# Kernel tuning notes

Measured on AMD Instinct MI355X. Metric: run time of the kernel, lower is better.

Reference implementation:

```python
import math
import jax, jax.numpy as jnp
import numpy as np

B = 2
TMAX = 1024
D = 1024
H = 16
DK = D // H
F = 4096
L = 2
CHUNK = 128
LEFT = 128
RIGHT = 32
EPS = 1e-5


def _build_mask(t_max, chunk, left, right):
    """Replicates EmformerEncoder.create_mask with audio_lens == t_max.
    Returns bool [T, T] where True = masked (disallowed), T = total_right + t_max."""
    num_chunks = math.ceil(t_max / chunk)
    ub = (num_chunks - 1) * right
    body = np.zeros((t_max, t_max), np.float32)
    mleft = np.zeros((t_max, ub), np.float32)
    mdiag = np.zeros((ub, ub), np.float32)
    mright = np.zeros((ub, t_max), np.float32)
    right_indexes = []
    for i in range(num_chunks):
        left_off = max(chunk * i - left, 0)
        start = chunk * i
        end = min(chunk * (i + 1), t_max)
        body[start:end, left_off:end] = 1
        if i == num_chunks - 1:
            break
        rem = t_max - (end + right)
        trl = right if rem >= 0 else t_max - end
        ri = len(right_indexes)
        mleft[start:start + chunk, ri:ri + trl] = 1
        mdiag[ri:ri + trl, ri:ri + trl] = 1
        mright[ri:ri + trl, left_off:end] = 1
        right_indexes += list(range(end, end + trl))
    rs = len(right_indexes)
    mleft = mleft[:, :rs]
    mdiag = mdiag[:rs, :rs]
    mright = mright[:rs, :]
    top = np.concatenate([mdiag, mright], axis=-1)
    bot = np.concatenate([mleft, body], axis=-1)
    m = np.concatenate([top, bot], axis=0)
    return m == 0  # True where attention is NOT allowed


def setup_inputs() -> dict:
    key = jax.random.key(0)
    ks = jax.random.split(key, 8)
    mask2d = _build_mask(TMAX, CHUNK, LEFT, RIGHT)  # [T, T]
    T = mask2d.shape[0]  # 1248
    w = lambda k, shape: jax.random.normal(k, shape, jnp.float32) * 0.02
    inp = {
        "input": jax.random.normal(ks[0], (B, T, D), jnp.float32),
        "ln_in_scale": jnp.ones((L, D), jnp.float32),
        "ln_in_bias": jnp.zeros((L, D), jnp.float32),
        "Wq": w(ks[1], (L, D, D)), "bq": jnp.zeros((L, D), jnp.float32),
        "Wk": w(ks[2], (L, D, D)), "bk": jnp.zeros((L, D), jnp.float32),
        "Wv": w(ks[3], (L, D, D)), "bv": jnp.zeros((L, D), jnp.float32),
        "ln1_scale": jnp.ones((L, D), jnp.float32),
        "ln1_bias": jnp.zeros((L, D), jnp.float32),
        "W1": w(ks[4], (L, D, F)), "b1": jnp.zeros((L, F), jnp.float32),
        "W2": w(ks[5], (L, F, D)), "b2": jnp.zeros((L, D), jnp.float32),
        "ln2_scale": jnp.ones((L, D), jnp.float32),
        "ln2_bias": jnp.zeros((L, D), jnp.float32),
        "mask": jnp.asarray(np.broadcast_to(mask2d[None, None], (B, 1, T, T)).copy()),
    }
    return inp


def _ln(x, scale, bias):
    m = jnp.mean(x, axis=-1, keepdims=True)
    v = jnp.mean(jnp.square(x - m), axis=-1, keepdims=True)
    return (x - m) * jax.lax.rsqrt(v + EPS) * scale + bias


def reference(input, ln_in_scale, ln_in_bias, Wq, bq, Wk, bk, Wv, bv,
              ln1_scale, ln1_bias, W1, b1, W2, b2, ln2_scale, ln2_bias, mask):
    x = input
    Bx, T, _ = x.shape
    scale = 1.0 / math.sqrt(DK)
    for l in range(L):
        h = _ln(x, ln_in_scale[l], ln_in_bias[l])  # pre-LN input (also residual base)
        q = (h @ Wq[l] + bq[l]).reshape(Bx, T, H, DK)
        k = (h @ Wk[l] + bk[l]).reshape(Bx, T, H, DK)
        v = (h @ Wv[l] + bv[l]).reshape(Bx, T, H, DK)
        scores = jnp.einsum('bqhd,bkhd->bhqk', q, k) * scale  # [B,H,T,T]
        scores = jnp.where(mask, -jnp.inf, scores)
        probs = jax.nn.softmax(scores, axis=-1)
        probs = jnp.where(mask, 0.0, probs)  # dropout_attn=0 -> identity
        o = jnp.einsum('bhqk,bkhd->bqhd', probs, v).reshape(Bx, T, D)
        attn_out = o + h
        y = _ln(attn_out, ln1_scale[l], ln1_bias[l])
        y = y @ W1[l] + b1[l]          # note: no activation in original code
        y = y @ W2[l] + b2[l] + attn_out
        x = _ln(y, ln2_scale[l], ln2_bias[l])
    return x
```

## Files before the change

kernel.cpp:

```cpp
#include <hip/hip_runtime.h>
#include <stdint.h>

typedef __attribute__((ext_vector_type(8))) short short8;
typedef __attribute__((ext_vector_type(4))) float f32x4;

#define DEV __device__ __forceinline__

DEV float bits2f(uint32_t u){ union{uint32_t u;float f;}v; v.u=u; return v.f; }
DEV float bf1(uint16_t s){ return bits2f(((uint32_t)s)<<16); }
DEV uint16_t f2bf(float f){ union{float f;uint32_t u;}v; v.f=f; uint32_t u=v.u;
  return (uint16_t)((u + 0x7fffu + ((u>>16)&1u))>>16); }
DEV uint16_t f2h(float a){ union{_Float16 h; uint16_t u;}v; v.h=(_Float16)a; return v.u; }
DEV float h2f(uint16_t s){ union{uint16_t u; _Float16 h;}v; v.u=s; return (float)v.h; }

DEV float ldval(const float* p, size_t i){ return p[i]; }
DEV float ldval(const uint16_t* p, size_t i){ return bf1(p[i]); }
DEV void stval(float* p, size_t i, float v){ p[i]=v; }
DEV void stval(uint16_t* p, size_t i, float v){ p[i]=f2bf(v); }

DEV void async16(const void* g, void* l){
#if __has_builtin(__builtin_amdgcn_global_load_lds)
  __builtin_amdgcn_global_load_lds((const __attribute__((address_space(1))) void*)g,
                                   (__attribute__((address_space(3))) void*)l, 16, 0, 0);
#else
  int lane = threadIdx.x & 63;
  *(uint4*)((char*)l + lane*16) = *(const uint4*)((const char*)g);
#endif
}

template<int TM, int TN, bool SPLIT>
__global__ __launch_bounds__(256) void gemm_t(
    const uint16_t* __restrict__ A, const uint16_t* __restrict__ Bt,
    const float* __restrict__ bias, void* __restrict__ Cout,
    int N, int K, int kchunk, int gm, int gx, int gy, int nG,
    const float* __restrict__ Tsrc1, const float* __restrict__ Tsrc2,
    uint16_t* __restrict__ Tdst1, uint16_t* __restrict__ Tdst2) {
  __shared__ uint16_t sA[3][TM*32];
  __shared__ uint16_t sB[3][TN*32];
  constexpr int LPS = TM/64 + TN/64;
  const int tid = threadIdx.x;
  const int lin = blockIdx.y*gx + blockIdx.x;

  if (lin >= nG) {
    float (*t)[33] = (float(*)[33])&sA[0][0];
    int tt = lin - nG;
    const float* src; uint16_t* dst; int R, C, c0, r0;
    if (tt < 4096) { src = Tsrc1; dst = Tdst1; R = 1024; C = 4096;
                     c0 = (tt&127)*32; r0 = (tt>>7)*32; }
    else { tt -= 4096; src = Tsrc2; dst = Tdst2; R = 4096; C = 1024;
           c0 = (tt&31)*32; r0 = (tt>>5)*32; }
    const int tx = tid&31, ty = tid>>5;
    #pragma unroll
    for (int i=0;i<4;i++) t[ty+8*i][tx] = src[(size_t)(r0+ty+8*i)*C + c0+tx];
    __syncthreads();
    #pragma unroll
    for (int i=0;i<4;i++) dst[(size_t)(c0+ty+8*i)*R + r0+tx] = f2bf(t[tx][ty+8*i]);
    return;
  }

  int mt_, nt_;
  if (gm > 0) {
    const int xcd = lin & 7, idx = lin >> 3;
    const int RM = gy / gm;
    const int RN = (gx * gm) >> 3;
    const int rm = xcd % gm, rn = xcd / gm;
    mt_ = rm*RM + idx % RM;
    nt_ = rn*RN + idx / RM;
  } else {
    const int q8 = (gx*gy) >> 3;
    const int swz = (lin & 7)*q8 + (lin >> 3);
    mt_ = swz % gy; nt_ = swz / gy;
  }
  const int m0 = mt_*TM, n0 = nt_*TN;
  const int kb = SPLIT ? blockIdx.z*kchunk : 0;
  const int kend = SPLIT ? kb + kchunk : K;
  const int wid = tid>>6, lane = tid&63;
  constexpr int WM = TM/2, MT = WM/16;
  constexpr int WN = TN/2, NT = WN/16;
  const int wm = (wid&1)*WM, wn = (wid>>1)*WN;
  f32x4 acc[MT][NT];
  #pragma unroll
  for (int a=0;a<MT;a++)
    #pragma unroll
    for (int b=0;b<NT;b++) acc[a][b] = (f32x4){0.f,0.f,0.f,0.f};
  const int lrow = lane>>2;
  const int lcol = (((lane&3) ^ ((lrow>>1)&3)))*8;
  const int fr = lane&15, fc = lane>>4;
  const int rsw = (fc ^ ((fr>>1)&3))*8;

  auto stage = [&](int buf, int k0) {
    #pragma unroll
    for (int j = 0; j < TM/64; ++j) {
      int r0 = wid*(TM/4) + j*16;
      async16(A + (size_t)(m0+r0+lrow)*K + k0 + lcol, &sA[buf][r0*32]);
    }
    #pragma unroll
    for (int j = 0; j < TN/64; ++j) {
      int r0 = wid*(TN/4) + j*16;
      async16(Bt + (size_t)(n0+r0+lrow)*K + k0 + lcol, &sB[buf][r0*32]);
    }
  };

  const int niter = (kend - kb) >> 5;
  stage(0, kb);
  if (niter > 1) stage(1, kb + 32);
  int cur = 0;
  for (int it = 0; it < niter; ++it) {
    if (it+1 < niter) {
      if constexpr (LPS == 4)      asm volatile("s_waitcnt vmcnt(4)" ::: "memory");
      else if constexpr (LPS == 3) asm volatile("s_waitcnt vmcnt(3)" ::: "memory");
      else                         asm volatile("s_waitcnt vmcnt(2)" ::: "memory");
    } else {
      asm volatile("s_waitcnt vmcnt(0)" ::: "memory");
    }
    __builtin_amdgcn_s_barrier();
    __builtin_amdgcn_sched_barrier(0);
    if (it+2 < niter) {
      int b2 = cur+2; if (b2>=3) b2-=3;
      stage(b2, kb + (it+2)*32);
    }
    short8 af[MT], bfv[NT];
    #pragma unroll
    for (int t=0;t<MT;t++) af[t] = *(const short8*)&sA[cur][(wm + t*16 + fr)*32 + rsw];
    #pragma unroll
    for (int t=0;t<NT;t++) bfv[t] = *(const short8*)&sB[cur][(wn + t*16 + fr)*32 + rsw];
    #pragma unroll
    for (int mt=0;mt<MT;mt++)
      #pragma unroll
      for (int nt=0;nt<NT;nt++)
        acc[mt][nt] = __builtin_amdgcn_mfma_f32_16x16x32_bf16(af[mt], bfv[nt], acc[mt][nt], 0,0,0);
    if (++cur == 3) cur = 0;
  }
  const int cl = lane&15, rl = (lane>>4)*4;
  if (SPLIT) {
    float* Pz = (float*)Cout + (size_t)blockIdx.z*2560*N;
    #pragma unroll
    for (int nt=0;nt<NT;nt++) {
      int n = n0 + wn + nt*16 + cl;
      #pragma unroll
      for (int mt=0;mt<MT;mt++)
        #pragma unroll
        for (int r=0;r<4;r++)
          Pz[(size_t)(m0 + wm + mt*16 + rl + r)*N + n] = acc[mt][nt][r];
    }
  } else {
    uint16_t* C = (uint16_t*)Cout;
    #pragma unroll
    for (int nt=0;nt<NT;nt++) {
      int n = n0 + wn + nt*16 + cl;
      float bv = bias ? bias[n] : 0.f;
      #pragma unroll
      for (int mt=0;mt<MT;mt++)
        #pragma unroll
        for (int r=0;r<4;r++)
          C[(size_t)(m0 + wm + mt*16 + rl + r)*N + n] = f2bf(acc[mt][nt][r] + bv);
    }
  }
}

template<typename TI, typename TO>
DEV void ln_body(int row, int tid, const TI* x, const float* sc, const float* bi,
                 TO* out, float* red) {
  const size_t base = (size_t)row*1024 + tid*4;
  float v0=ldval(x,base), v1=ldval(x,base+1), v2=ldval(x,base+2), v3=ldval(x,base+3);
  float s = v0+v1+v2+v3;
  float sq = v0*v0+v1*v1+v2*v2+v3*v3;
  #pragma unroll
  for (int off=32; off; off>>=1){ s += __shfl_xor(s,off); sq += __shfl_xor(sq,off); }
  int wid=tid>>6, lane=tid&63;
  if (lane==0){ red[wid]=s; red[4+wid]=sq; }
  __syncthreads();
  s = red[0]+red[1]+red[2]+red[3]; sq = red[4]+red[5]+red[6]+red[7];
  float mean = s*(1.f/1024.f);
  float inv  = rsqrtf(sq*(1.f/1024.f) - mean*mean + 1e-5f);
  int c = tid*4;
  stval(out, base,   (v0-mean)*inv*sc[c]   + bi[c]);
  stval(out, base+1, (v1-mean)*inv*sc[c+1] + bi[c+1]);
  stval(out, base+2, (v2-mean)*inv*sc[c+2] + bi[c+2]);
  stval(out, base+3, (v3-mean)*inv*sc[c+3] + bi[c+3]);
}

template<typename TI, typename TO>
__global__ __launch_bounds__(256) void ln_k(const TI* __restrict__ x,
    const float* __restrict__ sc, const float* __restrict__ bi,
    TO* __restrict__ out) {
  __shared__ float red[8];
  ln_body<TI,TO>(blockIdx.x, threadIdx.x, x, sc, bi, out, red);
}

template<typename TO>
__global__ __launch_bounds__(256) void ln2_fused(const float* __restrict__ P,
    const float* __restrict__ b2, const uint16_t* __restrict__ resid,
    const float* __restrict__ sc, const float* __restrict__ bi,
    TO* __restrict__ out) {
  const int row = blockIdx.x, tid = threadIdx.x;
  const size_t base = (size_t)row*1024 + tid*4;
  float4 p0 = *(const float4*)(P + base);
  float4 p1 = *(const float4*)(P + (size_t)2560*1024 + base);
  int c = tid*4;
  float v0 = p0.x+p1.x+b2[c]  +bf1(resid[base]);
  float v1 = p0.y+p1.y+b2[c+1]+bf1(resid[base+1]);
  float v2 = p0.z+p1.z+b2[c+2]+bf1(resid[base+2]);
  float v3 = p0.w+p1.w+b2[c+3]+bf1(resid[base+3]);
  float s = v0+v1+v2+v3;
  float sq = v0*v0+v1*v1+v2*v2+v3*v3;
  #pragma unroll
  for (int off=32; off; off>>=1){ s += __shfl_xor(s,off); sq += __shfl_xor(sq,off); }
  __shared__ float red[8];
  int wid=tid>>6, lane=tid&63;
  if (lane==0){ red[wid]=s; red[4+wid]=sq; }
  __syncthreads();
  s = red[0]+red[1]+red[2]+red[3]; sq = red[4]+red[5]+red[6]+red[7];
  float mean = s*(1.f/1024.f);
  float inv  = rsqrtf(sq*(1.f/1024.f) - mean*mean + 1e-5f);
  stval(out, base,   (v0-mean)*inv*sc[c]   + bi[c]);
  stval(out, base+1, (v1-mean)*inv*sc[c+1] + bi[c+1]);
  stval(out, base+2, (v2-mean)*inv*sc[c+2] + bi[c+2]);
  stval(out, base+3, (v3-mean)*inv*sc[c+3] + bi[c+3]);
}

__global__ __launch_bounds__(256) void attn_fused(
    const uint32_t* __restrict__ qkv32, const uint16_t* __restrict__ hres,
    uint16_t* __restrict__ attn_out) {
  const int blk = blockIdx.x;
  const int qg = (blk>>3)&3;
  const int g  = (blk&7) + ((blk>>5)<<3);
  const int ci = g&7, hh = (g>>3)&15, bb = g>>7;
  const int sum_cnt = (ci<7)?32:0;
  const int bstart = (ci>=1)?128*(ci-1):0;
  const int bend = (ci==7)?1024:128*(ci+1);
  const int nk = sum_cnt + (bend - bstart);
  const int rowbase = bb*1248;
  const int tid = threadIdx.x, wid = tid>>6, lane = tid&63;
  const int fr = lane&15, fc = lane>>4;

  __shared__ __attribute__((aligned(16))) uint16_t sm[30848];
  uint16_t* SP16 = sm;
  uint16_t* Q16 = sm + 20736;
  uint32_t* QD  = (uint32_t*)Q16;
  uint16_t* V16 = sm + 11840;
  uint32_t* VD  = (uint32_t*)(sm + 11840);

  for (int idx = tid; idx < 40*8; idx += 256) {
    int j = idx>>3, q4 = idx&7;
    int ql = qg*40 + j;
    int tq = (ql<32) ? (32*ci+ql) : (224+128*ci+ql-32);
    *(uint4*)&QD[j*36 + q4*4] =
      *(const uint4*)&qkv32[(size_t)(rowbase+tq)*1536 + hh*32 + q4*4];
  }
  __syncthreads();

  const int n_mt = nk>>4;
  const int qoff[3] = {0,16,24};
  f32x4 accs[5][3];
  #pragma unroll
  for (int a=0;a<5;a++)
    #pragma unroll
    for (int b=0;b<3;b++) accs[a][b] = (f32x4){0.f,0.f,0.f,0.f};
  __builtin_amdgcn_s_setprio(1);
  #pragma unroll
  for (int ks=0; ks<2; ++ks) {
    short8 bq_[3];
    #pragma unroll
    for (int nt=0;nt<3;nt++)
      bq_[nt] = *(const short8*)&Q16[(qoff[nt]+fr)*72 + ks*32 + fc*8];
    #pragma unroll
    for (int t=0;t<5;t++) {
      int mt = wid + 4*t;
      if (mt < n_mt) {
        int mrow = mt*16 + fr;
        int tk = (mrow < sum_cnt) ? (32*ci + mrow) : (224 + bstart + mrow - sum_cnt);
        short8 a_ = *(const short8*)&qkv32[(size_t)(rowbase+tk)*1536 + 512 + hh*32 + ks*16 + fc*4];
        #pragma unroll
        for (int nt=0;nt<3;nt++)
          accs[t][nt] = __builtin_amdgcn_mfma_f32_16x16x32_bf16(a_, bq_[nt], accs[t][nt], 0,0,0);
      }
    }
  }
  __builtin_amdgcn_s_setprio(0);
  __syncthreads();

  #pragma unroll
  for (int t=0;t<5;t++) {
    int mt = wid + 4*t;
    if (mt < n_mt) {
      #pragma unroll
      for (int nt=0;nt<3;nt++) {
        int q = qoff[nt] + fr;
        #pragma unroll
        for (int r=0;r<4;r++)
          SP16[q*296 + mt*16 + fc*4 + r] = f2h(accs[t][nt][r]*0.125f);
      }
    }
  }
  for (int idx = tid; idx < nk*8; idx += 256) {
    int j = idx>>3, q4 = idx&7;
    int tk = (j < sum_cnt) ? (32*ci + j) : (224 + bstart + (j - sum_cnt));
    uint4 w = *(const uint4*)&qkv32[(size_t)(rowbase+tk)*1536 + 1024 + hh*32 + q4*4];
    uint32_t* dst = &VD[j*33 + q4*4];
    dst[0]=w.x; dst[1]=w.y; dst[2]=w.z; dst[3]=w.w;
  }
  __syncthreads();

  for (int i=0;i<10;i++) {
    int row = wid*10 + i;
    float v[5];
    #pragma unroll
    for (int g2=0;g2<5;g2++){ int k=g2*64+lane; v[g2] = (k<nk) ? h2f(SP16[row*296+k]) : -1e30f; }
    float mx = fmaxf(fmaxf(fmaxf(v[0],v[1]),fmaxf(v[2],v[3])),v[4]);
    #pragma unroll
    for (int off=32; off; off>>=1) mx = fmaxf(mx, __shfl_xor(mx,off));
    float p[5], sum=0.f;
    #pragma unroll
    for (int g2=0;g2<5;g2++){ p[g2] = __expf(v[g2]-mx); if (g2*64+lane>=nk) p[g2]=0.f; sum+=p[g2]; }
    #pragma unroll
    for (int off=32; off; off>>=1) sum += __shfl_xor(sum,off);
    float inv = 1.f/sum;
    #pragma unroll
    for (int g2=0;g2<5;g2++){ int k=g2*64+lane; if (k<nk) SP16[row*296+k] = f2bf(p[g2]*inv); }
  }
  __syncthreads();

  const int nkt = nk>>5;
  f32x4 acco[3];
  #pragma unroll
  for (int t=0;t<3;t++) acco[t] = (f32x4){0.f,0.f,0.f,0.f};
  const uint16_t* vcol = V16 + wid*16 + fr;
  __builtin_amdgcn_s_setprio(1);
  for (int kt=0; kt<nkt; ++kt) {
    short8 bv_;
    #pragma unroll
    for (int j=0;j<8;j++) bv_[j] = (short)vcol[(kt*32 + fc*8 + j)*66];
    #pragma unroll
    for (int t=0;t<3;t++) {
      short8 a_ = *(const short8*)&SP16[(qoff[t]+fr)*296 + kt*32 + fc*8];
      acco[t] = __builtin_amdgcn_mfma_f32_16x16x32_bf16(a_, bv_, acco[t], 0,0,0);
    }
  }
  __builtin_amdgcn_s_setprio(0);
  #pragma unroll
  for (int t=0;t<3;t++) {
    #pragma unroll
    for (int r=0;r<4;r++) {
      bool vq = true;
      if (ci==7 && qg==0 && (qoff[t]+fc*4+r)<32) vq = false;
      if (vq) {
        int qll = qg*40 + qoff[t] + fc*4 + r;
        int tq = (qll<32) ? (32*ci+qll) : (224+128*ci+qll-32);
        size_t addr = (size_t)(rowbase+tq)*1024 + hh*64 + wid*16 + fr;
        attn_out[addr] = f2bf(acco[t][r] + bf1(hres[addr]));
      }
    }
  }
}

__global__ void prep_k(const float* __restrict__ Wq, const float* __restrict__ Wk,
                       const float* __restrict__ Wv, const float* __restrict__ bq,
                       const float* __restrict__ bk, const float* __restrict__ bv,
                       uint16_t* __restrict__ wt_qkv, float* __restrict__ bqkv,
                       const void* __restrict__ lnx, int lnx_f32,
                       const float* __restrict__ lnsc, const float* __restrict__ lnbi,
                       uint16_t* __restrict__ lnout) {
  __shared__ float t[32][33];
  const int blk = blockIdx.x;
  const int tx = threadIdx.x, ty = threadIdx.y;
  if (blk >= 3084) {
    int row = blk - 3084;
    int tid = ty*32 + tx;
    float* red = &t[0][0];
    if (lnx_f32) ln_body<float,uint16_t>((int)row, tid, (const float*)lnx, lnsc, lnbi, lnout, red);
    else         ln_body<uint16_t,uint16_t>((int)row, tid, (const uint16_t*)lnx, lnsc, lnbi, lnout, red);
    return;
  }
  if (blk >= 3072) {
    int i = (blk-3072)*256 + ty*32 + tx;
    bqkv[i] = (i<1024) ? bq[i] : ((i<2048) ? bk[i-1024] : bv[i-2048]);
    return;
  }
  int w = blk>>10, tt = blk&1023;
  const float* src = (w==0)?Wq:((w==1)?Wk:Wv);
  uint16_t* dst = wt_qkv + (size_t)w*1048576;
  const int R = 1024, C = 1024;
  const int c0 = (tt&31)*32, r0 = (tt>>5)*32;
  #pragma unroll
  for (int i=0;i<4;i++) t[ty+8*i][tx] = src[(size_t)(r0+ty+8*i)*C + c0+tx];
  __syncthreads();
  #pragma unroll
  for (int i=0;i<4;i++) dst[(size_t)(c0+ty+8*i)*R + r0+tx] = f2bf(t[tx][ty+8*i]);
}

extern "C" void kernel_launch(void* const* d_in, const int* in_sizes, int n_in,
                              void* d_out, int out_size, void* d_ws, size_t ws_size,
                              hipStream_t stream) {
  const float* input  = (const float*)d_in[0];
  const float* lnin_s = (const float*)d_in[1];
  const float* lnin_b = (const float*)d_in[2];
  const float* Wq = (const float*)d_in[3];
  const float* bq = (const float*)d_in[4];
  const float* Wk = (const float*)d_in[5];
  const float* bk = (const float*)d_in[6];
  const float* Wv = (const float*)d_in[7];
  const float* bv = (const float*)d_in[8];
  const float* ln1_s = (const float*)d_in[9];
  const float* ln1_b = (const float*)d_in[10];
  const float* W1 = (const float*)d_in[11];
  const float* b1 = (const float*)d_in[12];
  const float* W2 = (const float*)d_in[13];
  const float* b2 = (const float*)d_in[14];
  const float* ln2_s = (const float*)d_in[15];
  const float* ln2_b = (const float*)d_in[16];

  char* ws = (char*)d_ws;
  uint16_t* wt_qkv = (uint16_t*)(ws + 0);
  uint16_t* wt_w1  = (uint16_t*)(ws + 6291456);
  uint16_t* wt_w2  = (uint16_t*)(ws + 14680064);
  float*    bqkv   = (float*)   (ws + 23068672);
  uint16_t* hbuf   = (uint16_t*)(ws + 23080960);
  uint16_t* qkvb   = (uint16_t*)(ws + 28323840);
  uint16_t* attnb  = (uint16_t*)(ws + 44052480);
  uint16_t* zbuf   = (uint16_t*)(ws + 49295360);
  float*    pbuf   = (float*)   (ws + 54538240);
  uint16_t* y1b    = hbuf;
  uint16_t* x1b    = zbuf;

  const uint16_t* xcur_bf = x1b;
  for (int l=0; l<2; ++l) {
    prep_k<<<5580, dim3(32,8), 0, stream>>>(Wq+(size_t)l*1048576, Wk+(size_t)l*1048576,
        Wv+(size_t)l*1048576, bq+l*1024, bk+l*1024, bv+l*1024, wt_qkv, bqkv,
        (l==0) ? (const void*)input : (const void*)xcur_bf, (l==0)?1:0,
        lnin_s+l*1024, lnin_b+l*1024, hbuf);

    gemm_t<128,128,false><<<dim3(8672),256,0,stream>>>(hbuf, wt_qkv, bqkv, qkvb,
        3072, 1024, 0, 2, 24, 20, 480,
        W1+(size_t)l*4194304, W2+(size_t)l*4194304, wt_w1, wt_w2);
    attn_fused<<<1024,256,0,stream>>>((const uint32_t*)qkvb, hbuf, attnb);
    ln_k<uint16_t,uint16_t><<<2496,256,0,stream>>>(attnb, ln1_s+l*1024, ln1_b+l*1024, zbuf);
    gemm_t<128,128,false><<<dim3(32,20),256,0,stream>>>(zbuf, wt_w1, b1+l*4096, y1b,
        4096, 1024, 0, 2, 32, 20, 640, nullptr, nullptr, nullptr, nullptr);
    gemm_t<128,64,true><<<dim3(16,20,2),256,0,stream>>>(y1b, wt_w2, nullptr, pbuf,
        1024, 4096, 2048, 0, 16, 20, 320, nullptr, nullptr, nullptr, nullptr);
    if (l==1) ln2_fused<float>   <<<2496,256,0,stream>>>(pbuf, b2+l*1024, attnb, ln2_s+l*1024, ln2_b+l*1024, (float*)d_out);
    else      ln2_fused<uint16_t><<<2496,256,0,stream>>>(pbuf, b2+l*1024, attnb, ln2_s+l*1024, ln2_b+l*1024, x1b);
  }
  (void)in_sizes; (void)n_in; (void)out_size; (void)ws_size;
}
```

Before: 481.6 us.

## Unroll layers, fuse LN2 with next input LN, overlap QKV weight prep with W1 GEMM

Unrolls the two-layer loop so layer 0's output LayerNorm and layer 1's input LayerNorm run in one kernel, skipping the bf16 write and reread of the intermediate x. Layer 1's QKV weight transpose and bias packing become extra blocks of layer 0's W1 GEMM launch, which removes the separate prep launch and overlaps that work with the GEMM. The GEMM kernel gains a mode flag and more arguments. Intermediate x is no longer rounded to bf16 before the second LayerNorm.

```diff
diff --git a/kernel.cpp b/kernel.cpp
--- a/kernel.cpp
+++ b/kernel.cpp
@@ -32,9 +32,12 @@
 __global__ __launch_bounds__(256) void gemm_t(
     const uint16_t* __restrict__ A, const uint16_t* __restrict__ Bt,
     const float* __restrict__ bias, void* __restrict__ Cout,
-    int N, int K, int kchunk, int gm, int gx, int gy, int nG,
+    int N, int K, int kchunk, int gm, int gx, int gy, int nG, int tmode,
     const float* __restrict__ Tsrc1, const float* __restrict__ Tsrc2,
-    uint16_t* __restrict__ Tdst1, uint16_t* __restrict__ Tdst2) {
+    const float* __restrict__ Tsrc3,
+    uint16_t* __restrict__ Tdst1, uint16_t* __restrict__ Tdst2,
+    const float* __restrict__ Bq, const float* __restrict__ Bk,
+    const float* __restrict__ Bv, float* __restrict__ bqv) {
   __shared__ uint16_t sA[3][TM*32];
   __shared__ uint16_t sB[3][TN*32];
   constexpr int LPS = TM/64 + TN/64;
@@ -45,10 +48,22 @@
     float (*t)[33] = (float(*)[33])&sA[0][0];
     int tt = lin - nG;
     const float* src; uint16_t* dst; int R, C, c0, r0;
-    if (tt < 4096) { src = Tsrc1; dst = Tdst1; R = 1024; C = 4096;
-                     c0 = (tt&127)*32; r0 = (tt>>7)*32; }
-    else { tt -= 4096; src = Tsrc2; dst = Tdst2; R = 4096; C = 1024;
-           c0 = (tt&31)*32; r0 = (tt>>5)*32; }
+    if (tmode == 0) {
+      if (tt < 4096) { src = Tsrc1; dst = Tdst1; R = 1024; C = 4096;
+                       c0 = (tt&127)*32; r0 = (tt>>7)*32; }
+      else { tt -= 4096; src = Tsrc2; dst = Tdst2; R = 4096; C = 1024;
+             c0 = (tt&31)*32; r0 = (tt>>5)*32; }
+    } else {
+      if (tt >= 3072) {
+        int i = (tt-3072)*256 + tid;
+        bqv[i] = (i<1024) ? Bq[i] : ((i<2048) ? Bk[i-1024] : Bv[i-2048]);
+        return;
+      }
+      int w = tt>>10, t2 = tt&1023;
+      src = (w==0)?Tsrc1:((w==1)?Tsrc2:Tsrc3);
+      dst = Tdst1 + (size_t)w*1048576;
+      R = 1024; C = 1024; c0 = (t2&31)*32; r0 = (t2>>5)*32;
+    }
     const int tx = tid&31, ty = tid>>5;
     #pragma unroll
     for (int i=0;i<4;i++) t[ty+8*i][tx] = src[(size_t)(r0+ty+8*i)*C + c0+tx];
@@ -219,6 +234,51 @@
   stval(out, base+3, (v3-mean)*inv*sc[c+3] + bi[c+3]);
 }
 
+__global__ __launch_bounds__(256) void ln2ln_fused(const float* __restrict__ P,
+    const float* __restrict__ b2, const uint16_t* __restrict__ resid,
+    const float* __restrict__ sc2, const float* __restrict__ bi2,
+    const float* __restrict__ sci, const float* __restrict__ bii,
+    uint16_t* __restrict__ hout) {
+  const int row = blockIdx.x, tid = threadIdx.x;
+  const size_t base = (size_t)row*1024 + tid*4;
+  float4 p0 = *(const float4*)(P + base);
+  float4 p1 = *(const float4*)(P + (size_t)2560*1024 + base);
+  int c = tid*4;
+  float v0 = p0.x+p1.x+b2[c]  +bf1(resid[base]);
+  float v1 = p0.y+p1.y+b2[c+1]+bf1(resid[base+1]);
+  float v2 = p0.z+p1.z+b2[c+2]+bf1(resid[base+2]);
+  float v3 = p0.w+p1.w+b2[c+3]+bf1(resid[base+3]);
+  float s = v0+v1+v2+v3;
+  float sq = v0*v0+v1*v1+v2*v2+v3*v3;
+  #pragma unroll
+  for (int off=32; off; off>>=1){ s += __shfl_xor(s,off); sq += __shfl_xor(sq,off); }
+  __shared__ float red[8];
+  int wid=tid>>6, lane=tid&63;
+  if (lane==0){ red[wid]=s; red[4+wid]=sq; }
+  __syncthreads();
+  s = red[0]+red[1]+red[2]+red[3]; sq = red[4]+red[5]+red[6]+red[7];
+  float mean = s*(1.f/1024.f);
+  float inv  = rsqrtf(sq*(1.f/1024.f) - mean*mean + 1e-5f);
+  float x0 = (v0-mean)*inv*sc2[c]   + bi2[c];
+  float x1 = (v1-mean)*inv*sc2[c+1] + bi2[c+1];
+  float x2 = (v2-mean)*inv*sc2[c+2] + bi2[c+2];
+  float x3 = (v3-mean)*inv*sc2[c+3] + bi2[c+3];
+  float s2 = x0+x1+x2+x3;
+  float q2 = x0*x0+x1*x1+x2*x2+x3*x3;
+  #pragma unroll
+  for (int off=32; off; off>>=1){ s2 += __shfl_xor(s2,off); q2 += __shfl_xor(q2,off); }
+  __syncthreads();
+  if (lane==0){ red[wid]=s2; red[4+wid]=q2; }
+  __syncthreads();
+  s2 = red[0]+red[1]+red[2]+red[3]; q2 = red[4]+red[5]+red[6]+red[7];
+  float mean2 = s2*(1.f/1024.f);
+  float inv2  = rsqrtf(q2*(1.f/1024.f) - mean2*mean2 + 1e-5f);
+  hout[base]   = f2bf((x0-mean2)*inv2*sci[c]   + bii[c]);
+  hout[base+1] = f2bf((x1-mean2)*inv2*sci[c+1] + bii[c+1]);
+  hout[base+2] = f2bf((x2-mean2)*inv2*sci[c+2] + bii[c+2]);
+  hout[base+3] = f2bf((x3-mean2)*inv2*sci[c+3] + bii[c+3]);
+}
+
 __global__ __launch_bounds__(256) void attn_fused(
     const uint32_t* __restrict__ qkv32, const uint16_t* __restrict__ hres,
     uint16_t* __restrict__ attn_out) {
@@ -358,7 +418,7 @@
                        const float* __restrict__ Wv, const float* __restrict__ bq,
                        const float* __restrict__ bk, const float* __restrict__ bv,
                        uint16_t* __restrict__ wt_qkv, float* __restrict__ bqkv,
-                       const void* __restrict__ lnx, int lnx_f32,
+                       const float* __restrict__ lnx,
                        const float* __restrict__ lnsc, const float* __restrict__ lnbi,
                        uint16_t* __restrict__ lnout) {
   __shared__ float t[32][33];
@@ -368,8 +428,7 @@
     int row = blk - 3084;
     int tid = ty*32 + tx;
     float* red = &t[0][0];
-    if (lnx_f32) ln_body<float,uint16_t>((int)row, tid, (const float*)lnx, lnsc, lnbi, lnout, red);
-    else         ln_body<uint16_t,uint16_t>((int)row, tid, (const uint16_t*)lnx, lnsc, lnbi, lnout, red);
+    ln_body<float,uint16_t>((int)row, tid, lnx, lnsc, lnbi, lnout, red);
     return;
   }
   if (blk >= 3072) {
@@ -421,26 +480,38 @@
   uint16_t* zbuf   = (uint16_t*)(ws + 49295360);
   float*    pbuf   = (float*)   (ws + 54538240);
   uint16_t* y1b    = hbuf;
-  uint16_t* x1b    = zbuf;
-
-  const uint16_t* xcur_bf = x1b;
-  for (int l=0; l<2; ++l) {
-    prep_k<<<5580, dim3(32,8), 0, stream>>>(Wq+(size_t)l*1048576, Wk+(size_t)l*1048576,
-        Wv+(size_t)l*1048576, bq+l*1024, bk+l*1024, bv+l*1024, wt_qkv, bqkv,
-        (l==0) ? (const void*)input : (const void*)xcur_bf, (l==0)?1:0,
-        lnin_s+l*1024, lnin_b+l*1024, hbuf);
-
-    gemm_t<128,128,false><<<dim3(8672),256,0,stream>>>(hbuf, wt_qkv, bqkv, qkvb,
-        3072, 1024, 0, 2, 24, 20, 480,
-        W1+(size_t)l*4194304, W2+(size_t)l*4194304, wt_w1, wt_w2);
-    attn_fused<<<1024,256,0,stream>>>((const uint32_t*)qkvb, hbuf, attnb);
-    ln_k<uint16_t,uint16_t><<<2496,256,0,stream>>>(attnb, ln1_s+l*1024, ln1_b+l*1024, zbuf);
-    gemm_t<128,128,false><<<dim3(32,20),256,0,stream>>>(zbuf, wt_w1, b1+l*4096, y1b,
-        4096, 1024, 0, 2, 32, 20, 640, nullptr, nullptr, nullptr, nullptr);
-    gemm_t<128,64,true><<<dim3(16,20,2),256,0,stream>>>(y1b, wt_w2, nullptr, pbuf,
-        1024, 4096, 2048, 0, 16, 20, 320, nullptr, nullptr, nullptr, nullptr);
-    if (l==1) ln2_fused<float>   <<<2496,256,0,stream>>>(pbuf, b2+l*1024, attnb, ln2_s+l*1024, ln2_b+l*1024, (float*)d_out);
-    else      ln2_fused<uint16_t><<<2496,256,0,stream>>>(pbuf, b2+l*1024, attnb, ln2_s+l*1024, ln2_b+l*1024, x1b);
-  }
+
+  prep_k<<<5580, dim3(32,8), 0, stream>>>(Wq, Wk, Wv, bq, bk, bv, wt_qkv, bqkv,
+      input, lnin_s, lnin_b, hbuf);
+
+  gemm_t<128,128,false><<<dim3(8672),256,0,stream>>>(hbuf, wt_qkv, bqkv, qkvb,
+      3072, 1024, 0, 2, 24, 20, 480, 0,
+      W1, W2, nullptr, wt_w1, wt_w2, nullptr, nullptr, nullptr, nullptr);
+  attn_fused<<<1024,256,0,stream>>>((const uint32_t*)qkvb, hbuf, attnb);
+  ln_k<uint16_t,uint16_t><<<2496,256,0,stream>>>(attnb, ln1_s, ln1_b, zbuf);
+  gemm_t<128,128,false><<<dim3(3724),256,0,stream>>>(zbuf, wt_w1, b1, y1b,
+      4096, 1024, 0, 2, 32, 20, 640, 1,
+      Wq+1048576, Wk+1048576, Wv+1048576, wt_qkv, nullptr,
+      bq+1024, bk+1024, bv+1024, bqkv);
+  gemm_t<128,64,true><<<dim3(16,20,2),256,0,stream>>>(y1b, wt_w2, nullptr, pbuf,
+      1024, 4096, 2048, 0, 16, 20, 320, 0,
+      nullptr, nullptr, nullptr, nullptr, nullptr, nullptr, nullptr, nullptr, nullptr);
+  ln2ln_fused<<<2496,256,0,stream>>>(pbuf, b2, attnb, ln2_s, ln2_b,
+      lnin_s+1024, lnin_b+1024, hbuf);
+
+  gemm_t<128,128,false><<<dim3(8672),256,0,stream>>>(hbuf, wt_qkv, bqkv, qkvb,
+      3072, 1024, 0, 2, 24, 20, 480, 0,
+      W1+4194304, W2+4194304, nullptr, wt_w1, wt_w2, nullptr, nullptr, nullptr, nullptr);
+  attn_fused<<<1024,256,0,stream>>>((const uint32_t*)qkvb, hbuf, attnb);
+  ln_k<uint16_t,uint16_t><<<2496,256,0,stream>>>(attnb, ln1_s+1024, ln1_b+1024, zbuf);
+  gemm_t<128,128,false><<<dim3(32,20),256,0,stream>>>(zbuf, wt_w1, b1+4096, y1b,
+      4096, 1024, 0, 2, 32, 20, 640, 0,
+      nullptr, nullptr, nullptr, nullptr, nullptr, nullptr, nullptr, nullptr, nullptr);
+  gemm_t<128,64,true><<<dim3(16,20,2),256,0,stream>>>(y1b, wt_w2, nullptr, pbuf,
+      1024, 4096, 2048, 0, 16, 20, 320, 0,
+      nullptr, nullptr, nullptr, nullptr, nullptr, nullptr, nullptr, nullptr, nullptr);
+  ln2_fused<float><<<2496,256,0,stream>>>(pbuf, b2+1024, attnb, ln2_s+1024, ln2_b+1024,
+      (float*)d_out);
+
   (void)in_sizes; (void)n_in; (void)out_size; (void)ws_size;
 }
```

Measured after the change: 471.7 us. 2.1% less time.
